# Kernel tuning notes

Hardware: AMD Instinct MI355X
Metric: run time of the kernel (lower is better)

## Reference

```python
import jax, jax.numpy as jnp
import numpy as np
from jax import lax

N_NODES = 116
N_EDGES = 1160
D_FEAT = 653  # SAGEConv in/out channels (last dim)


def _sage_max(x, src, dst, w_l, w_r, b):
    # PyG SAGEConv(aggr='max'): out = lin_l(max_j x_j) + lin_r(x)
    # x: [N, C, F]; aggregation over incoming edges per target node.
    msgs = x[src]  # [E, C, F]
    agg = jax.ops.segment_max(msgs, dst, num_segments=N_NODES)
    agg = jnp.where(jnp.isfinite(agg), agg, 0.0)  # empty segments -> 0 (PyG behavior)
    return jnp.einsum('ncf,gf->ncg', agg, w_l) + b + jnp.einsum('ncf,gf->ncg', x, w_r)


def setup_inputs() -> dict:
    key = jax.random.key(0)
    ks = jax.random.split(key, 16)
    inp = {}
    inp['x'] = jax.random.normal(ks[0], (N_NODES, 64, 657), dtype=jnp.float32)
    inp['edge_index'] = jax.random.randint(ks[1], (2, N_EDGES), 0, N_NODES, dtype=jnp.int64)
    # Conv1d(64 -> 256, kernel=5, groups=4): weight [256, 16, 5]
    inp['conv_w'] = jax.random.normal(ks[2], (256, 16, 5), dtype=jnp.float32) * 0.05
    inp['conv_b'] = jax.random.normal(ks[3], (256,), dtype=jnp.float32) * 0.05
    s = 1.0 / np.sqrt(D_FEAT)
    inp['sage_wl'] = jax.random.normal(ks[4], (D_FEAT, D_FEAT), dtype=jnp.float32) * s
    inp['sage_wr'] = jax.random.normal(ks[5], (D_FEAT, D_FEAT), dtype=jnp.float32) * s
    inp['sage_b'] = jnp.zeros((D_FEAT,), dtype=jnp.float32)
    inp['fc1_w'] = jax.random.normal(ks[6], (128, D_FEAT), dtype=jnp.float32) * s
    inp['fc1_b'] = jnp.zeros((128,), dtype=jnp.float32)
    inp['fc2_w'] = jax.random.normal(ks[7], (32, 128), dtype=jnp.float32) * (1.0 / np.sqrt(128))
    inp['fc2_b'] = jnp.zeros((32,), dtype=jnp.float32)
    inp['fc3_w'] = jax.random.normal(ks[8], (4, 32), dtype=jnp.float32) * (1.0 / np.sqrt(32))
    inp['fc3_b'] = jnp.zeros((4,), dtype=jnp.float32)
    return inp


def reference(x, edge_index, conv_w, conv_b, sage_wl, sage_wr, sage_b,
              fc1_w, fc1_b, fc2_w, fc2_b, fc3_w, fc3_b):
    # grouped Conv1d: [N,64,657] -> [N,256,653]
    h = lax.conv_general_dilated(
        x, conv_w, window_strides=(1,), padding='VALID',
        dimension_numbers=('NCH', 'OIH', 'NCH'), feature_group_count=4)
    h = h + conv_b[None, :, None]
    src, dst = edge_index[0], edge_index[1]
    for _ in range(3):  # same SAGEConv layer applied three times
        h = _sage_max(h, src, dst, sage_wl, sage_wr, sage_b)
    # global_mean_pool over the single graph (batch all zeros) then squeeze
    h = h.mean(axis=0)  # [256, 653]
    h = jax.nn.gelu(h @ fc1_w.T + fc1_b, approximate=False)
    h = jax.nn.gelu(h @ fc2_w.T + fc2_b, approximate=False)
    h = h @ fc3_w.T + fc3_b  # [256, 4]
    return jax.nn.softmax(h, axis=1)
```

## Files before the change

### kernel.cpp

```cpp
#include <hip/hip_runtime.h>
#include <hip/hip_bf16.h>
#include <math.h>

#define NN 116
#define NE 1160
#define CCH 256
#define FF 653
#define KP 672
#define MM (NN*CCH)
#define NPAD 768
#define NT6 (NPAD/128)
#define NKS (2*KP/32)
#define SZH ((size_t)MM*KP)

typedef unsigned short ushort;
typedef short bf16x8 __attribute__((ext_vector_type(8)));
typedef float f32x4 __attribute__((ext_vector_type(4)));

__device__ __forceinline__ float bfbits_to_f(ushort u) {
    unsigned int w = ((unsigned int)u) << 16;
    return __uint_as_float(w);
}
__device__ __forceinline__ ushort f_to_bfbits(float f) {
    unsigned int u = __float_as_uint(f);
    u += 0x7FFFu + ((u >> 16) & 1u);
    return (ushort)(u >> 16);
}

__device__ __forceinline__ void gl_lds16(const void* g, void* l) {
    __builtin_amdgcn_global_load_lds(
        (const __attribute__((address_space(1))) unsigned int*)g,
        (__attribute__((address_space(3))) unsigned int*)l, 16, 0, 0);
}

__global__ void build_csr_k(const int* __restrict__ ei, int* __restrict__ off,
                            int* __restrict__ lst) {
    __shared__ int s_cnt[NN];
    __shared__ int s_off[NN + 1];
    int t = threadIdx.x;
    for (int i = t; i < NN; i += blockDim.x) s_cnt[i] = 0;
    __syncthreads();
    for (int e = t; e < NE; e += blockDim.x) atomicAdd(&s_cnt[ei[NE + e]], 1);
    __syncthreads();
    if (t == 0) {
        s_off[0] = 0;
        for (int i = 0; i < NN; ++i) s_off[i + 1] = s_off[i] + s_cnt[i];
    }
    __syncthreads();
    for (int i = t; i < NN; i += blockDim.x) { off[i] = s_off[i]; s_cnt[i] = 0; }
    if (t == 0) off[NN] = s_off[NN];
    __syncthreads();
    for (int e = t; e < NE; e += blockDim.x) {
        int d = ei[NE + e];
        int p = atomicAdd(&s_cnt[d], 1);
        lst[s_off[d] + p] = ei[e];
    }
}

__global__ void build_wc_k(const float* __restrict__ wl, const float* __restrict__ wr,
                           ushort* __restrict__ wc) {
    int idx = blockIdx.x * 256 + threadIdx.x;
    const int total = 2 * NPAD * KP;
    if (idx >= total) return;
    int k = idx % KP;
    int rem = idx / KP;
    int n = rem % NPAD;
    int p = rem / NPAD;
    float v = 0.f;
    if (n < FF && k < FF) v = (p ? wr : wl)[(size_t)n * FF + k];
    wc[idx] = f_to_bfbits(v);
}

__global__ __launch_bounds__(256) void conv1d_k(
    const float* __restrict__ x, const float* __restrict__ w,
    const float* __restrict__ b, ushort* __restrict__ h) {
    const int f  = blockIdx.x * 256 + threadIdx.x;
    if (f >= KP) return;
    const int n  = blockIdx.y;
    const int o0 = blockIdx.z * 16;
    const int g  = o0 >> 6;
    if (f >= FF) {
#pragma unroll
        for (int oo = 0; oo < 16; ++oo)
            h[(size_t)(n * CCH + o0 + oo) * KP + f] = 0;
        return;
    }
    const float* xp = x + ((size_t)n * 64 + g * 16) * 657 + f;
    const float* wq = w + o0 * 80;
    float acc[16];
#pragma unroll
    for (int oo = 0; oo < 16; ++oo) acc[oo] = b[o0 + oo];
#pragma unroll
    for (int i = 0; i < 16; ++i) {
        float xv[5];
#pragma unroll
        for (int k = 0; k < 5; ++k) xv[k] = xp[i * 657 + k];
#pragma unroll
        for (int oo = 0; oo < 16; ++oo) {
            const float* wp = wq + oo * 80 + i * 5;
            acc[oo] = fmaf(xv[0], wp[0], acc[oo]);
            acc[oo] = fmaf(xv[1], wp[1], acc[oo]);
            acc[oo] = fmaf(xv[2], wp[2], acc[oo]);
            acc[oo] = fmaf(xv[3], wp[3], acc[oo]);
            acc[oo] = fmaf(xv[4], wp[4], acc[oo]);
        }
    }
#pragma unroll
    for (int oo = 0; oo < 16; ++oo)
        h[(size_t)(n * CCH + o0 + oo) * KP + f] = f_to_bfbits(acc[oo]);
}

__global__ __launch_bounds__(256) void seg_maxT_k(
    const ushort* __restrict__ h, ushort* __restrict__ agg,
    const int* __restrict__ off, const int* __restrict__ lst) {
    __shared__ uint4 sh[NN * 4];
    const int c  = blockIdx.x;
    const int f0 = blockIdx.y * 32;
    const int t  = threadIdx.x;
    for (int u = t; u < NN * 4; u += 256) {
        int n = u >> 2, sub = u & 3;
        sh[u] = *(const uint4*)(h + ((size_t)(n * CCH + c)) * KP + f0 + sub * 8);
    }
    __syncthreads();
    for (int u = t; u < NN * 4; u += 256) {
        int n = u >> 2, sub = u & 3;
        int o0 = off[n], o1 = off[n + 1];
        uint4 outv;
        if (o0 == o1) {
            outv = make_uint4(0, 0, 0, 0);
        } else {
            float m[8];
#pragma unroll
            for (int i = 0; i < 8; ++i) m[i] = -3.4e38f;
            for (int e = o0; e < o1; ++e) {
                int s = lst[e];
                uint4 v = sh[s * 4 + sub];
                unsigned int uu[4] = {v.x, v.y, v.z, v.w};
#pragma unroll
                for (int q = 0; q < 4; ++q) {
                    float lo = __uint_as_float(uu[q] << 16);
                    float hi = __uint_as_float(uu[q] & 0xFFFF0000u);
                    m[2*q]   = fmaxf(m[2*q],   lo);
                    m[2*q+1] = fmaxf(m[2*q+1], hi);
                }
            }
            unsigned int o[4];
#pragma unroll
            for (int q = 0; q < 4; ++q) {
                unsigned int a  = __float_as_uint(m[2*q])   >> 16;
                unsigned int bq = __float_as_uint(m[2*q+1]) & 0xFFFF0000u;
                o[q] = a | bq;
            }
            outv = make_uint4(o[0], o[1], o[2], o[3]);
        }
        *(uint4*)(agg + ((size_t)(n * CCH + c)) * KP + f0 + sub * 8) = outv;
    }
}

__global__ __launch_bounds__(256) void seg_pool2_k(
    const ushort* __restrict__ h, ushort* __restrict__ aggP,
    ushort* __restrict__ h2P,
    const int* __restrict__ off, const int* __restrict__ lst) {
    __shared__ uint4 sh[NN * 4];
    __shared__ float pm[NN][32];
    const int c  = blockIdx.x;
    const int f0 = blockIdx.y * 32;
    const int t  = threadIdx.x;
    for (int u = t; u < NN * 4; u += 256) {
        int n = u >> 2, sub = u & 3;
        sh[u] = *(const uint4*)(h + ((size_t)(n * CCH + c)) * KP + f0 + sub * 8);
    }
    __syncthreads();
    for (int u = t; u < NN * 4; u += 256) {
        int n = u >> 2, sub = u & 3;
        int o0 = off[n], o1 = off[n + 1];
        float m[8];
        if (o0 == o1) {
#pragma unroll
            for (int i = 0; i < 8; ++i) m[i] = 0.f;
        } else {
#pragma unroll
            for (int i = 0; i < 8; ++i) m[i] = -3.4e38f;
            for (int e = o0; e < o1; ++e) {
                int s = lst[e];
                uint4 v = sh[s * 4 + sub];
                unsigned int uu[4] = {v.x, v.y, v.z, v.w};
#pragma unroll
                for (int q = 0; q < 4; ++q) {
                    float lo = __uint_as_float(uu[q] << 16);
                    float hi = __uint_as_float(uu[q] & 0xFFFF0000u);
                    m[2*q]   = fmaxf(m[2*q],   lo);
                    m[2*q+1] = fmaxf(m[2*q+1], hi);
                }
            }
#pragma unroll
            for (int i = 0; i < 8; ++i)
                m[i] = __uint_as_float(__float_as_uint(m[i]) & 0xFFFF0000u);
        }
#pragma unroll
        for (int i = 0; i < 8; ++i) pm[n][sub * 8 + i] = m[i];
    }
    __syncthreads();
    if (t < 32) {
        const float inv = 1.0f / NN;
        float sa = 0.f, s2 = 0.f;
        for (int n = 0; n < NN; ++n) {
            sa += pm[n][t];
            uint4 v = sh[n * 4 + (t >> 3)];
            unsigned int w = ((const unsigned int*)&v)[(t >> 1) & 3];
            float hv = (t & 1) ? __uint_as_float(w & 0xFFFF0000u)
                               : __uint_as_float(w << 16);
            s2 += hv;
        }
        aggP[(size_t)c * KP + f0 + t] = f_to_bfbits(sa * inv);
        h2P [(size_t)c * KP + f0 + t] = f_to_bfbits(s2 * inv);
    }
}

__global__ __launch_bounds__(256) void sage_gemm_k(
    const ushort* __restrict__ Agg, const ushort* __restrict__ Hcur,
    const ushort* __restrict__ Wc, const float* __restrict__ bias,
    ushort* __restrict__ Hnxt)
{
    __shared__ ushort As[2][128 * 32];
    __shared__ ushort Bs[2][128 * 32];
    const int bid = blockIdx.x;
    const int nwg = gridDim.x;
    const int q   = nwg >> 3, r = nwg & 7;
    const int xcd = bid & 7,  jj = bid >> 3;
    const int wgid = (xcd < r ? xcd * (q + 1) : r * (q + 1) + (xcd - r) * q) + jj;
    const int mt = wgid / NT6;
    const int nt = wgid - mt * NT6;
    const int bm = mt * 128;
    const int bn = nt * 128;
    const int tid  = threadIdx.x;
    const int lane = tid & 63;
    const int wid  = tid >> 6;
    const int wm = (wid >> 1) * 64;
    const int wn = (wid & 1) * 64;

    f32x4 acc[4][4];
#pragma unroll
    for (int i = 0; i < 4; ++i)
#pragma unroll
        for (int j = 0; j < 4; ++j) acc[i][j] = 0.f;

    const int srow   = lane >> 2;
    const int schunk = lane & 3;
    const int schk   = (schunk ^ ((srow >> 1) & 3)) * 8;
    const int lr  = lane & 15;
    const int cc  = lane >> 4;
    const int kc  = (cc ^ ((lr >> 1) & 3)) * 8;
    const int ldsoff = wid * 16 * 32;

#define STAGE(b, kk) do {                                                     \
        int _kk = (kk);                                                       \
        const ushort* _Ab = (_kk < 21) ? Agg : Hcur;                          \
        const ushort* _Wb = Wc + (size_t)(_kk < 21 ? 0 : 1) * NPAD * KP;      \
        int _k0 = (_kk < 21 ? _kk : _kk - 21) * 32;                           \
        const ushort* _ga = _Ab + (size_t)(bm + wid * 16 + srow) * KP + _k0 + schk; \
        const ushort* _gb = _Wb + (size_t)(bn + wid * 16 + srow) * KP + _k0 + schk; \
        gl_lds16(_ga, &As[b][ldsoff]);                                        \
        gl_lds16(_ga + (size_t)64 * KP, &As[b][ldsoff + 64 * 32]);            \
        gl_lds16(_gb, &Bs[b][ldsoff]);                                        \
        gl_lds16(_gb + (size_t)64 * KP, &Bs[b][ldsoff + 64 * 32]);            \
    } while (0)

#define COMPUTE(b) do {                                                       \
        bf16x8 _af[4], _bf[4];                                                \
        _Pragma("unroll")                                                     \
        for (int i = 0; i < 4; ++i)                                           \
            _af[i] = *(const bf16x8*)&As[b][(wm + i * 16 + lr) * 32 + kc];    \
        _Pragma("unroll")                                                     \
        for (int j = 0; j < 4; ++j)                                           \
            _bf[j] = *(const bf16x8*)&Bs[b][(wn + j * 16 + lr) * 32 + kc];    \
        _Pragma("unroll")                                                     \
        for (int i = 0; i < 4; ++i)                                           \
            _Pragma("unroll")                                                 \
            for (int j = 0; j < 4; ++j)                                       \
                acc[i][j] = __builtin_amdgcn_mfma_f32_16x16x32_bf16(          \
                    _af[i], _bf[j], acc[i][j], 0, 0, 0);                      \
    } while (0)

    STAGE(0, 0);
    __syncthreads();
#pragma unroll 1
    for (int kk = 0; kk < NKS; kk += 2) {
        STAGE(1, kk + 1);
        COMPUTE(0);
        __syncthreads();
        if (kk + 2 < NKS) STAGE(0, kk + 2);
        COMPUTE(1);
        __syncthreads();
    }
#undef STAGE
#undef COMPUTE

    const int lg = lane >> 4;
#pragma unroll
    for (int j = 0; j < 4; ++j) {
        int n = bn + wn + j * 16 + lr;
        if (n >= KP) continue;
        bool valid = n < FF;
        float bv = valid ? bias[n] : 0.f;
#pragma unroll
        for (int i = 0; i < 4; ++i) {
#pragma unroll
            for (int rgi = 0; rgi < 4; ++rgi) {
                int m = bm + wm + i * 16 + lg * 4 + rgi;
                float v = valid ? (acc[i][j][rgi] + bv) : 0.f;
                Hnxt[(size_t)m * KP + n] = f_to_bfbits(v);
            }
        }
    }
}

__device__ __forceinline__ float gelu_exact(float v) {
    return 0.5f * v * (1.0f + erff(v * 0.70710678118654752f));
}

__global__ void head_k(const ushort* __restrict__ pool,
                       const float* __restrict__ w1, const float* __restrict__ b1,
                       const float* __restrict__ w2, const float* __restrict__ b2,
                       const float* __restrict__ w3, const float* __restrict__ b3,
                       float* __restrict__ out) {
    __shared__ float row[FF];
    __shared__ float h1[128];
    __shared__ float h2[32];
    __shared__ float sc[4];
    const int c = blockIdx.x;
    const int t = threadIdx.x;
    for (int i = t; i < FF; i += 128) row[i] = bfbits_to_f(pool[(size_t)c * KP + i]);
    __syncthreads();
    {
        const float* wp = w1 + (size_t)t * FF;
        float s = b1[t];
        for (int i = 0; i < FF; ++i) s = fmaf(row[i], wp[i], s);
        h1[t] = gelu_exact(s);
    }
    __syncthreads();
    if (t < 32) {
        const float* wp = w2 + (size_t)t * 128;
        float s = b2[t];
#pragma unroll
        for (int i = 0; i < 128; ++i) s = fmaf(h1[i], wp[i], s);
        h2[t] = gelu_exact(s);
    }
    __syncthreads();
    if (t < 4) {
        const float* wp = w3 + (size_t)t * 32;
        float s = b3[t];
#pragma unroll
        for (int i = 0; i < 32; ++i) s = fmaf(h2[i], wp[i], s);
        sc[t] = s;
    }
    __syncthreads();
    if (t < 4) {
        float mx = fmaxf(fmaxf(sc[0], sc[1]), fmaxf(sc[2], sc[3]));
        float e0 = __expf(sc[0] - mx), e1 = __expf(sc[1] - mx);
        float e2 = __expf(sc[2] - mx), e3 = __expf(sc[3] - mx);
        float inv = 1.0f / (e0 + e1 + e2 + e3);
        float ev = (t == 0) ? e0 : (t == 1) ? e1 : (t == 2) ? e2 : e3;
        out[(size_t)c * 4 + t] = ev * inv;
    }
}

extern "C" void kernel_launch(void* const* d_in, const int* in_sizes, int n_in,
                              void* d_out, int out_size, void* d_ws, size_t ws_size,
                              hipStream_t stream) {
    const float* x      = (const float*)d_in[0];
    const int*   ei     = (const int*)  d_in[1];
    const float* conv_w = (const float*)d_in[2];
    const float* conv_b = (const float*)d_in[3];
    const float* wl     = (const float*)d_in[4];
    const float* wr     = (const float*)d_in[5];
    const float* sb     = (const float*)d_in[6];
    const float* fc1w   = (const float*)d_in[7];
    const float* fc1b   = (const float*)d_in[8];
    const float* fc2w   = (const float*)d_in[9];
    const float* fc2b   = (const float*)d_in[10];
    const float* fc3w   = (const float*)d_in[11];
    const float* fc3b   = (const float*)d_in[12];
    float* out = (float*)d_out;

    ushort* hA   = (ushort*)d_ws;
    ushort* hB   = hA + SZH;
    ushort* agg  = hB + SZH;
    ushort* wc   = agg + SZH;
    ushort* aggP = wc + (size_t)2 * NPAD * KP;
    ushort* h2P  = aggP + (size_t)CCH * KP;
    ushort* poolt= h2P + (size_t)CCH * KP;
    int*    off  = (int*)(poolt + (size_t)CCH * KP);
    int*    lst  = off + 128;

    build_csr_k<<<1, 256, 0, stream>>>(ei, off, lst);
    build_wc_k<<<(2 * NPAD * KP + 255) / 256, 256, 0, stream>>>(wl, wr, wc);
    {
        dim3 cgrid(3, NN, 16);
        conv1d_k<<<cgrid, 256, 0, stream>>>(x, conv_w, conv_b, hA);
    }

    dim3 tg(CCH, KP / 32);
    seg_maxT_k<<<tg, 256, 0, stream>>>(hA, agg, off, lst);
    sage_gemm_k<<<MM / 128 * NT6, 256, 0, stream>>>(agg, hA, wc, sb, hB);
    seg_maxT_k<<<tg, 256, 0, stream>>>(hB, agg, off, lst);
    sage_gemm_k<<<MM / 128 * NT6, 256, 0, stream>>>(agg, hB, wc, sb, hA);
    seg_pool2_k<<<tg, 256, 0, stream>>>(hA, aggP, h2P, off, lst);
    sage_gemm_k<<<(CCH / 128) * NT6, 256, 0, stream>>>(aggP, h2P, wc, sb, poolt);
    head_k<<<CCH, 128, 0, stream>>>(poolt, fc1w, fc1b, fc2w, fc2b, fc3w, fc3b, out);
}
```

Baseline: 594.1 us.

## Deepen SAGE GEMM LDS pipeline to four buffers with explicit vmcnt waits

```diff
diff --git a/kernel.cpp b/kernel.cpp
--- a/kernel.cpp
+++ b/kernel.cpp
@@ -222,8 +222,8 @@
     const ushort* __restrict__ Wc, const float* __restrict__ bias,
     ushort* __restrict__ Hnxt)
 {
-    __shared__ ushort As[2][128 * 32];
-    __shared__ ushort Bs[2][128 * 32];
+    __shared__ ushort As[4][128 * 32];
+    __shared__ ushort Bs[4][128 * 32];
     const int bid = blockIdx.x;
     const int nwg = gridDim.x;
     const int q   = nwg >> 3, r = nwg & 7;
@@ -253,17 +253,18 @@
     const int kc  = (cc ^ ((lr >> 1) & 3)) * 8;
     const int ldsoff = wid * 16 * 32;
 
-#define STAGE(b, kk) do {                                                     \
+#define STAGE(kk) do {                                                        \
         int _kk = (kk);                                                       \
+        int _b  = _kk & 3;                                                    \
         const ushort* _Ab = (_kk < 21) ? Agg : Hcur;                          \
         const ushort* _Wb = Wc + (size_t)(_kk < 21 ? 0 : 1) * NPAD * KP;      \
         int _k0 = (_kk < 21 ? _kk : _kk - 21) * 32;                           \
         const ushort* _ga = _Ab + (size_t)(bm + wid * 16 + srow) * KP + _k0 + schk; \
         const ushort* _gb = _Wb + (size_t)(bn + wid * 16 + srow) * KP + _k0 + schk; \
-        gl_lds16(_ga, &As[b][ldsoff]);                                        \
-        gl_lds16(_ga + (size_t)64 * KP, &As[b][ldsoff + 64 * 32]);            \
-        gl_lds16(_gb, &Bs[b][ldsoff]);                                        \
-        gl_lds16(_gb + (size_t)64 * KP, &Bs[b][ldsoff + 64 * 32]);            \
+        gl_lds16(_ga, &As[_b][ldsoff]);                                       \
+        gl_lds16(_ga + (size_t)64 * KP, &As[_b][ldsoff + 64 * 32]);           \
+        gl_lds16(_gb, &Bs[_b][ldsoff]);                                       \
+        gl_lds16(_gb + (size_t)64 * KP, &Bs[_b][ldsoff + 64 * 32]);           \
     } while (0)
 
 #define COMPUTE(b) do {                                                       \
@@ -282,16 +283,21 @@
                     _af[i], _bf[j], acc[i][j], 0, 0, 0);                      \
     } while (0)
 
-    STAGE(0, 0);
-    __syncthreads();
+    STAGE(0);
+    STAGE(1);
 #pragma unroll 1
-    for (int kk = 0; kk < NKS; kk += 2) {
-        STAGE(1, kk + 1);
-        COMPUTE(0);
-        __syncthreads();
-        if (kk + 2 < NKS) STAGE(0, kk + 2);
-        COMPUTE(1);
-        __syncthreads();
+    for (int kk = 0; kk < NKS; ++kk) {
+        if (kk + 2 < NKS) {
+            STAGE(kk + 2);
+            asm volatile("s_waitcnt vmcnt(8)" ::: "memory");
+        } else if (kk + 1 < NKS) {
+            asm volatile("s_waitcnt vmcnt(4)" ::: "memory");
+        } else {
+            asm volatile("s_waitcnt vmcnt(0)" ::: "memory");
+        }
+        __builtin_amdgcn_s_barrier();
+        __builtin_amdgcn_sched_barrier(0);
+        COMPUTE(kk & 3);
     }
 #undef STAGE
 #undef COMPUTE
```

Result: no change. 598.1 us (+0.7%).

## Stage conv1d input group in shared memory and reuse across output channels

Applied to the files above, without the earlier changes.

```diff
diff --git a/kernel.cpp b/kernel.cpp
--- a/kernel.cpp
+++ b/kernel.cpp
@@ -74,40 +74,55 @@
 __global__ __launch_bounds__(256) void conv1d_k(
     const float* __restrict__ x, const float* __restrict__ w,
     const float* __restrict__ b, ushort* __restrict__ h) {
-    const int f  = blockIdx.x * 256 + threadIdx.x;
-    if (f >= KP) return;
-    const int n  = blockIdx.y;
-    const int o0 = blockIdx.z * 16;
-    const int g  = o0 >> 6;
-    if (f >= FF) {
-#pragma unroll
-        for (int oo = 0; oo < 16; ++oo)
-            h[(size_t)(n * CCH + o0 + oo) * KP + f] = 0;
-        return;
-    }
-    const float* xp = x + ((size_t)n * 64 + g * 16) * 657 + f;
+    __shared__ float sx[16 * 657 + 32];
+    const int n   = blockIdx.x;
+    const int g   = blockIdx.y;
+    const int tid = threadIdx.x;
+    const float* xg = x + ((size_t)n * 64 + g * 16) * 657;
+    for (int i = tid; i < 16 * 657; i += 256) sx[i] = xg[i];
+    if (tid < 32) sx[16 * 657 + tid] = 0.f;
+    __syncthreads();
+    const int wv   = __builtin_amdgcn_readfirstlane(tid >> 6);
+    const int lane = tid & 63;
+    const int o0   = g * 64 + wv * 16;
     const float* wq = w + o0 * 80;
-    float acc[16];
-#pragma unroll
-    for (int oo = 0; oo < 16; ++oo) acc[oo] = b[o0 + oo];
-#pragma unroll
-    for (int i = 0; i < 16; ++i) {
-        float xv[5];
-#pragma unroll
-        for (int k = 0; k < 5; ++k) xv[k] = xp[i * 657 + k];
-#pragma unroll
-        for (int oo = 0; oo < 16; ++oo) {
-            const float* wp = wq + oo * 80 + i * 5;
-            acc[oo] = fmaf(xv[0], wp[0], acc[oo]);
-            acc[oo] = fmaf(xv[1], wp[1], acc[oo]);
-            acc[oo] = fmaf(xv[2], wp[2], acc[oo]);
-            acc[oo] = fmaf(xv[3], wp[3], acc[oo]);
-            acc[oo] = fmaf(xv[4], wp[4], acc[oo]);
+    float bv[16];
+#pragma unroll
+    for (int oo = 0; oo < 16; ++oo) bv[oo] = b[o0 + oo];
+
+#pragma unroll 1
+    for (int fc = 0; fc < 11; ++fc) {
+        const int f = fc * 64 + lane;
+        float xv[80];
+#pragma unroll
+        for (int i = 0; i < 16; ++i)
+#pragma unroll
+            for (int k = 0; k < 5; ++k)
+                xv[i * 5 + k] = sx[i * 657 + f + k];
+        float acc[16];
+#pragma unroll
+        for (int oo = 0; oo < 16; ++oo) acc[oo] = bv[oo];
+#pragma unroll
+        for (int i = 0; i < 16; ++i)
+#pragma unroll
+            for (int oo = 0; oo < 16; ++oo) {
+                const float* wp = wq + oo * 80 + i * 5;
+                acc[oo] = fmaf(xv[i * 5 + 0], wp[0], acc[oo]);
+                acc[oo] = fmaf(xv[i * 5 + 1], wp[1], acc[oo]);
+                acc[oo] = fmaf(xv[i * 5 + 2], wp[2], acc[oo]);
+                acc[oo] = fmaf(xv[i * 5 + 3], wp[3], acc[oo]);
+                acc[oo] = fmaf(xv[i * 5 + 4], wp[4], acc[oo]);
+            }
+        if (f < FF) {
+#pragma unroll
+            for (int oo = 0; oo < 16; ++oo)
+                h[(size_t)(n * CCH + o0 + oo) * KP + f] = f_to_bfbits(acc[oo]);
+        } else if (f < KP) {
+#pragma unroll
+            for (int oo = 0; oo < 16; ++oo)
+                h[(size_t)(n * CCH + o0 + oo) * KP + f] = 0;
         }
     }
-#pragma unroll
-    for (int oo = 0; oo < 16; ++oo)
-        h[(size_t)(n * CCH + o0 + oo) * KP + f] = f_to_bfbits(acc[oo]);
 }
 
 __global__ __launch_bounds__(256) void seg_maxT_k(
@@ -396,7 +411,7 @@
     build_csr_k<<<1, 256, 0, stream>>>(ei, off, lst);
     build_wc_k<<<(2 * NPAD * KP + 255) / 256, 256, 0, stream>>>(wl, wr, wc);
     {
-        dim3 cgrid(3, NN, 16);
+        dim3 cgrid(NN, 4);
         conv1d_k<<<cgrid, 256, 0, stream>>>(x, conv_w, conv_b, hA);
     }
 
```

Result: slower. 663.3 us (+11.6%).

## Replace direct grouped conv1d with im2col plus bf16 MFMA GEMM

Applied to the files above, without the earlier changes.

```diff
diff --git a/kernel.cpp b/kernel.cpp
--- a/kernel.cpp
+++ b/kernel.cpp
@@ -12,6 +12,8 @@
 #define NT6 (NPAD/128)
 #define NKS (2*KP/32)
 #define SZH ((size_t)MM*KP)
+#define FPAD 768
+#define CK 128
 
 typedef unsigned short ushort;
 typedef short bf16x8 __attribute__((ext_vector_type(8)));
@@ -71,43 +73,107 @@
     wc[idx] = f_to_bfbits(v);
 }
 
-__global__ __launch_bounds__(256) void conv1d_k(
-    const float* __restrict__ x, const float* __restrict__ w,
-    const float* __restrict__ b, ushort* __restrict__ h) {
-    const int f  = blockIdx.x * 256 + threadIdx.x;
-    if (f >= KP) return;
-    const int n  = blockIdx.y;
-    const int o0 = blockIdx.z * 16;
-    const int g  = o0 >> 6;
-    if (f >= FF) {
-#pragma unroll
-        for (int oo = 0; oo < 16; ++oo)
-            h[(size_t)(n * CCH + o0 + oo) * KP + f] = 0;
-        return;
-    }
-    const float* xp = x + ((size_t)n * 64 + g * 16) * 657 + f;
-    const float* wq = w + o0 * 80;
-    float acc[16];
-#pragma unroll
-    for (int oo = 0; oo < 16; ++oo) acc[oo] = b[o0 + oo];
-#pragma unroll
-    for (int i = 0; i < 16; ++i) {
-        float xv[5];
-#pragma unroll
-        for (int k = 0; k < 5; ++k) xv[k] = xp[i * 657 + k];
-#pragma unroll
-        for (int oo = 0; oo < 16; ++oo) {
-            const float* wp = wq + oo * 80 + i * 5;
-            acc[oo] = fmaf(xv[0], wp[0], acc[oo]);
-            acc[oo] = fmaf(xv[1], wp[1], acc[oo]);
-            acc[oo] = fmaf(xv[2], wp[2], acc[oo]);
-            acc[oo] = fmaf(xv[3], wp[3], acc[oo]);
-            acc[oo] = fmaf(xv[4], wp[4], acc[oo]);
+__global__ void wb_k(const float* __restrict__ w, ushort* __restrict__ wb) {
+    int idx = blockIdx.x * 256 + threadIdx.x;
+    if (idx >= CCH * CK) return;
+    int k = idx & 127, o = idx >> 7;
+    int i = k >> 3, t = k & 7;
+    float v = (t < 5) ? w[o * 80 + i * 5 + t] : 0.f;
+    wb[idx] = f_to_bfbits(v);
+}
+
+__global__ __launch_bounds__(256) void im2col_k(const float* __restrict__ x,
+                                                ushort* __restrict__ xb) {
+    const int n = blockIdx.x, g = blockIdx.y;
+    const float* xg = x + ((size_t)n * 64 + g * 16) * 657;
+    ushort* slab = xb + ((size_t)(n * 4 + g)) * FPAD * CK;
+    for (int u = threadIdx.x; u < FF * 16; u += 256) {
+        int f = u >> 4, i = u & 15;
+        const float* xp = xg + i * 657 + f;
+        unsigned int e[5];
+#pragma unroll
+        for (int t = 0; t < 5; ++t) e[t] = f_to_bfbits(xp[t]);
+        uint4 v;
+        v.x = e[0] | (e[1] << 16);
+        v.y = e[2] | (e[3] << 16);
+        v.z = e[4];
+        v.w = 0u;
+        *(uint4*)(slab + (size_t)f * CK + i * 8) = v;
+    }
+}
+
+__global__ __launch_bounds__(256) void convgemm_k(
+    const ushort* __restrict__ xb, const ushort* __restrict__ wb,
+    const float* __restrict__ bias, ushort* __restrict__ h) {
+    __shared__ ushort As[2][64 * 32];
+    __shared__ ushort Bs[2][128 * 32];
+    const int bid   = blockIdx.x;
+    const int ftile = bid % 6;
+    const int rem   = bid / 6;
+    const int g     = rem & 3;
+    const int n     = rem >> 2;
+    const int tid = threadIdx.x, lane = tid & 63, wv = tid >> 6;
+    const int srow = lane >> 2, schunk = lane & 3;
+    const int schk = (schunk ^ ((srow >> 1) & 3)) * 8;
+    const int lr = lane & 15, cc = lane >> 4;
+    const int kc = (cc ^ ((lr >> 1) & 3)) * 8;
+    const int lg = lane >> 4;
+    const ushort* slab  = xb + ((size_t)(n * 4 + g)) * FPAD * CK;
+    const ushort* wbase = wb + (size_t)g * 64 * CK;
+
+    f32x4 acc[4][2];
+#pragma unroll
+    for (int i = 0; i < 4; ++i)
+#pragma unroll
+        for (int j = 0; j < 2; ++j) acc[i][j] = 0.f;
+
+#define CSTAGE(b, ks) do {                                                    \
+        int _k0 = (ks) * 32;                                                  \
+        const ushort* _ga = wbase + (size_t)(wv * 16 + srow) * CK + _k0 + schk; \
+        const ushort* _gb = slab + (size_t)(ftile * 128 + wv * 16 + srow) * CK + _k0 + schk; \
+        gl_lds16(_ga, &As[b][wv * 16 * 32]);                                  \
+        gl_lds16(_gb, &Bs[b][wv * 16 * 32]);                                  \
+        gl_lds16(_gb + (size_t)64 * CK, &Bs[b][wv * 16 * 32 + 64 * 32]);      \
+    } while (0)
+
+#define CCOMP(b) do {                                                         \
+        bf16x8 _af[4], _bf[2];                                                \
+        _Pragma("unroll")                                                     \
+        for (int i = 0; i < 4; ++i)                                           \
+            _af[i] = *(const bf16x8*)&As[b][(i * 16 + lr) * 32 + kc];         \
+        _Pragma("unroll")                                                     \
+        for (int j = 0; j < 2; ++j)                                           \
+            _bf[j] = *(const bf16x8*)&Bs[b][(wv * 32 + j * 16 + lr) * 32 + kc]; \
+        _Pragma("unroll")                                                     \
+        for (int i = 0; i < 4; ++i)                                           \
+            _Pragma("unroll")                                                 \
+            for (int j = 0; j < 2; ++j)                                       \
+                acc[i][j] = __builtin_amdgcn_mfma_f32_16x16x32_bf16(          \
+                    _af[i], _bf[j], acc[i][j], 0, 0, 0);                      \
+    } while (0)
+
+    CSTAGE(0, 0); __syncthreads();
+    CSTAGE(1, 1); CCOMP(0); __syncthreads();
+    CSTAGE(0, 2); CCOMP(1); __syncthreads();
+    CSTAGE(1, 3); CCOMP(0); __syncthreads();
+    CCOMP(1);
+#undef CSTAGE
+#undef CCOMP
+
+#pragma unroll
+    for (int i = 0; i < 4; ++i) {
+#pragma unroll
+        for (int j = 0; j < 2; ++j) {
+            int fl = ftile * 128 + wv * 32 + j * 16 + lr;
+            if (fl >= KP) continue;
+#pragma unroll
+            for (int r = 0; r < 4; ++r) {
+                int oa = g * 64 + i * 16 + lg * 4 + r;
+                float v = acc[i][j][r] + bias[oa];
+                h[(size_t)(n * CCH + oa) * KP + fl] = f_to_bfbits(v);
+            }
         }
     }
-#pragma unroll
-    for (int oo = 0; oo < 16; ++oo)
-        h[(size_t)(n * CCH + o0 + oo) * KP + f] = f_to_bfbits(acc[oo]);
 }
 
 __global__ __launch_bounds__(256) void seg_maxT_k(
@@ -390,15 +456,16 @@
     ushort* aggP = wc + (size_t)2 * NPAD * KP;
     ushort* h2P  = aggP + (size_t)CCH * KP;
     ushort* poolt= h2P + (size_t)CCH * KP;
-    int*    off  = (int*)(poolt + (size_t)CCH * KP);
+    ushort* wb   = poolt + (size_t)CCH * KP;
+    ushort* xb   = wb + (size_t)CCH * CK;
+    int*    off  = (int*)(xb + (size_t)NN * 4 * FPAD * CK);
     int*    lst  = off + 128;
 
     build_csr_k<<<1, 256, 0, stream>>>(ei, off, lst);
     build_wc_k<<<(2 * NPAD * KP + 255) / 256, 256, 0, stream>>>(wl, wr, wc);
-    {
-        dim3 cgrid(3, NN, 16);
-        conv1d_k<<<cgrid, 256, 0, stream>>>(x, conv_w, conv_b, hA);
-    }
+    wb_k<<<(CCH * CK + 255) / 256, 256, 0, stream>>>(conv_w, wb);
+    im2col_k<<<dim3(NN, 4), 256, 0, stream>>>(x, xb);
+    convgemm_k<<<NN * 4 * 6, 256, 0, stream>>>(xb, wb, conv_b, hA);
 
     dim3 tg(CCH, KP / 32);
     seg_maxT_k<<<tg, 256, 0, stream>>>(hA, agg, off, lst);
```

Result: slower. 627.5 us (+5.6%).
